# Performance work log

Hardware: AMD Instinct MI355X
Metric: run time of the kernel (lower is better)

## Reference

```python
import jax, jax.numpy as jnp
import numpy as np

B, S, D, H = 4, 1024, 1024, 16
DK = D // H


def setup_inputs() -> dict:
    key = jax.random.key(0)
    ks = jax.random.split(key, 13)
    s = 1.0 / np.sqrt(D)
    return {
        "query": jax.random.normal(ks[0], (B, S, D), jnp.float32),
        "key": jax.random.normal(ks[1], (B, S, D), jnp.float32),
        "value": jax.random.normal(ks[2], (B, S, D), jnp.float32),
        "mask": jax.random.randint(ks[3], (B, H, S, S), 0, 2).astype(bool),
        "Wq": jax.random.normal(ks[4], (D, D), jnp.float32) * s,
        "bq": jnp.zeros((D,), jnp.float32),
        "Wk": jax.random.normal(ks[5], (D, D), jnp.float32) * s,
        "bk": jnp.zeros((D,), jnp.float32),
        "Wv": jax.random.normal(ks[6], (D, D), jnp.float32) * s,
        "bv": jnp.zeros((D,), jnp.float32),
        "Wo": jax.random.normal(ks[7], (D, D), jnp.float32) * s,
        "bo": jnp.zeros((D,), jnp.float32),
    }


def reference(query, key, value, mask, Wq, bq, Wk, bk, Wv, bv, Wo, bo):
    b = query.shape[0]
    # QKV projections, split heads: [B,S,D] -> [B,H,S,DK]
    q = (query @ Wq + bq).reshape(b, -1, H, DK).transpose(0, 2, 1, 3)
    k = (key @ Wk + bk).reshape(b, -1, H, DK).transpose(0, 2, 1, 3)
    v = (value @ Wv + bv).reshape(b, -1, H, DK).transpose(0, 2, 1, 3)
    # scaled dot-product attention with explicit [B,H,Sq,Sk] scores
    scores = jnp.einsum("bhqd,bhkd->bhqk", q, k) / jnp.sqrt(jnp.float32(DK))
    scores = jnp.where(mask, -jnp.inf, scores)
    attn_weights = jax.nn.softmax(scores, axis=-1)
    attn_out = jnp.einsum("bhqk,bhkd->bhqd", attn_weights, v)
    # merge heads and project out; dropout is identity in eval mode
    attn_out = attn_out.transpose(0, 2, 1, 3).reshape(b, -1, D)
    out = attn_out @ Wo + bo
    return out, attn_weights
```

## Files before the change

kernel.cpp:

```cpp
#include <hip/hip_runtime.h>

typedef __attribute__((ext_vector_type(8))) __bf16   bf16x8;
typedef __attribute__((ext_vector_type(4))) __bf16   bf16x4;
typedef __attribute__((ext_vector_type(8))) _Float16 halfx8;
typedef __attribute__((ext_vector_type(4))) float    floatx4;
typedef __attribute__((ext_vector_type(4))) int      intx4;

#define S_  1024
#define D_  1024
#define H_  16
#define DK_ 64
#define B_  4
#define M_  4096

__device__ __forceinline__ void gload_lds16(const void* g, void* l) {
  __builtin_amdgcn_global_load_lds(
      (const __attribute__((address_space(1))) unsigned int*)g,
      (__attribute__((address_space(3))) unsigned int*)l, 16, 0, 0);
}

__global__ __launch_bounds__(256) void prep(
    const float* __restrict__ q, const float* __restrict__ k,
    const float* __restrict__ v, __bf16* __restrict__ X,
    const float* __restrict__ W0, const float* __restrict__ W1,
    const float* __restrict__ W2, const float* __restrict__ W3,
    __bf16* __restrict__ WT, const unsigned char* __restrict__ m,
    int* __restrict__ flag)
{
  __shared__ __align__(16) unsigned char shb[9216];
  const int bid = blockIdx.x;
  const int t = threadIdx.x;
  if (bid < 6144) {
    const int z = bid >> 11;
    const int bx = bid & 2047;
    const float* src = (z == 0) ? q : (z == 1) ? k : v;
    __bf16* dst = X + (size_t)z * 4194304;
    const size_t idx = ((size_t)bx * 256 + t) * 8;
    floatx4 a = *(const floatx4*)(src + idx);
    floatx4 b = *(const floatx4*)(src + idx + 4);
    bf16x8 o;
#pragma unroll
    for (int j = 0; j < 4; ++j) { o[j] = (__bf16)a[j]; o[4 + j] = (__bf16)b[j]; }
    *(bf16x8*)(dst + idx) = o;
  } else if (bid < 7168) {
    const int g = bid - 6144;
    const int z = g >> 8, yy = (g >> 4) & 15, xx = g & 15;
    const float* W = (z == 0) ? W0 : (z == 1) ? W1 : (z == 2) ? W2 : W3;
    __bf16* O = WT + (size_t)z * (D_ * (size_t)D_);
    __bf16* T = (__bf16*)shb;
    const int r0 = yy * 64, c0 = xx * 64;
#pragma unroll
    for (int it = 0; it < 4; ++it) {
      int idx = t * 4 + it * 1024;
      int r = idx >> 6, c = idx & 63;
      floatx4 a = *(const floatx4*)(W + (size_t)(r0 + r) * D_ + c0 + c);
      bf16x4 o;
#pragma unroll
      for (int j = 0; j < 4; ++j) o[j] = (__bf16)a[j];
      *(bf16x4*)(&T[r * 72 + c]) = o;
    }
    __syncthreads();
#pragma unroll
    for (int it = 0; it < 2; ++it) {
      int idx = t * 8 + it * 2048;
      int orow = idx >> 6, oc = idx & 63;
      bf16x8 vv;
#pragma unroll
      for (int j = 0; j < 8; ++j) vv[j] = T[(oc + j) * 72 + orow];
      *(bf16x8*)(O + (size_t)(c0 + orow) * D_ + (r0 + oc)) = vv;
    }
  } else {
    unsigned* sacc = (unsigned*)shb;
    unsigned acc = 0;
    for (int i = t; i < 4096; i += 256)
      if (i & 3) acc |= m[i];
    sacc[t] = acc;
    __syncthreads();
    if (t == 0) {
      unsigned tot = 0;
      for (int i = 0; i < 256; ++i) tot |= sacc[i];
      flag[0] = tot ? 1 : 0;
    }
  }
}

template <int MODE>
__device__ __forceinline__ void gemm_body(
    const __bf16* __restrict__ X, const __bf16* __restrict__ WT,
    const float* __restrict__ bias, void* __restrict__ outp, __bf16* sh,
    const int m0, const int n0)
{
  __bf16* As = sh;
  __bf16* Bs = sh + 128 * 64;
  const int t = threadIdx.x;
  const int w = t >> 6, lane = t & 63, quad = lane >> 4, cl = lane & 15;
  const int wm = w >> 1, wn = w & 1;
  const int srow = lane >> 3, scol = (lane & 7) * 8;

  floatx4 acc[4][4];
#pragma unroll
  for (int i = 0; i < 4; ++i)
#pragma unroll
    for (int j = 0; j < 4; ++j) acc[i][j] = (floatx4){0.f, 0.f, 0.f, 0.f};

  for (int kt = 0; kt < 16; ++kt) {
    const int k0 = kt * 64;
    __syncthreads();
#pragma unroll
    for (int it = 0; it < 4; ++it) {
      const int ch = it * 4 + w;
      gload_lds16(X  + (size_t)(m0 + ch * 8 + srow) * D_ + k0 + scol, As + ch * 512);
      gload_lds16(WT + (size_t)(n0 + ch * 8 + srow) * D_ + k0 + scol, Bs + ch * 512);
    }
    __syncthreads();
#pragma unroll
    for (int ks = 0; ks < 2; ++ks) {
      bf16x8 a[4], b[4];
#pragma unroll
      for (int mt = 0; mt < 4; ++mt)
        a[mt] = *(const bf16x8*)(&As[(wm * 64 + mt * 16 + cl) * 64 + ks * 32 + quad * 8]);
#pragma unroll
      for (int nt = 0; nt < 4; ++nt)
        b[nt] = *(const bf16x8*)(&Bs[(wn * 64 + nt * 16 + cl) * 64 + ks * 32 + quad * 8]);
#pragma unroll
      for (int mt = 0; mt < 4; ++mt)
#pragma unroll
        for (int nt = 0; nt < 4; ++nt)
          acc[mt][nt] = __builtin_amdgcn_mfma_f32_16x16x32_bf16(a[mt], b[nt], acc[mt][nt], 0, 0, 0);
    }
  }

  if (MODE <= 2) {
#pragma unroll
    for (int mt = 0; mt < 4; ++mt)
#pragma unroll
      for (int nt = 0; nt < 4; ++nt) {
        const int nl = n0 + wn * 64 + nt * 16 + cl;
        const float bv = bias[nl];
#pragma unroll
        for (int r = 0; r < 4; ++r) {
          const int ml = m0 + wm * 64 + mt * 16 + quad * 4 + r;
          float v = acc[mt][nt][r] + bv;
          if (MODE == 0) {
            ((float*)outp)[(size_t)ml * D_ + nl] = v;
          } else {
            if (MODE == 1) v *= 0.125f;
            const int bb = ml >> 10, ss = ml & 1023, hh = nl >> 6, dd = nl & 63;
            ((_Float16*)outp)[(size_t)((bb * H_ + hh) * S_ + ss) * DK_ + dd] = (_Float16)v;
          }
        }
      }
  } else {
    __syncthreads();
    __bf16* T = sh + w * (64 * 72);
    const int hbase = n0 + wn * 64;
#pragma unroll
    for (int mt = 0; mt < 4; ++mt)
#pragma unroll
      for (int nt = 0; nt < 4; ++nt) {
        const int nl = hbase + nt * 16 + cl;
        const float bv = bias[nl];
        const int dk = nt * 16 + cl;
#pragma unroll
        for (int r = 0; r < 4; ++r) {
          const int sl = mt * 16 + quad * 4 + r;
          T[dk * 72 + sl] = (__bf16)(acc[mt][nt][r] + bv);
        }
      }
    __syncthreads();
    const int bb = m0 >> 10;
    const int hh = hbase >> 6;
    __bf16* out = (__bf16*)outp;
#pragma unroll
    for (int i = 0; i < 8; ++i) {
      int idx = lane * 8 + i * 512;
      int dk = idx >> 6, sl = idx & 63;
      bf16x8 v = *(const bf16x8*)(&T[dk * 72 + sl]);
      int sg = (m0 & 1023) + wm * 64 + sl;
      *(bf16x8*)(out + (size_t)((bb * H_ + hh) * DK_ + dk) * S_ + sg) = v;
    }
  }
}

__global__ __launch_bounds__(256) void gemm_qkv(
    const __bf16* __restrict__ Xbf, const __bf16* __restrict__ wt,
    const float* __restrict__ bq, const float* __restrict__ bk,
    const float* __restrict__ bv,
    void* __restrict__ Qo, void* __restrict__ Ko, void* __restrict__ Vto)
{
  __shared__ __bf16 sh[18432];
  const int z = blockIdx.z;
  const int m0 = blockIdx.x * 128, n0 = blockIdx.y * 128;
  if (z == 0)      gemm_body<1>(Xbf,               wt,               bq, Qo,  sh, m0, n0);
  else if (z == 1) gemm_body<2>(Xbf + 4194304,     wt + 1048576,     bk, Ko,  sh, m0, n0);
  else             gemm_body<3>(Xbf + 2 * 4194304, wt + 2 * 1048576, bv, Vto, sh, m0, n0);
}

__global__ __launch_bounds__(256) void gemm_out(
    const __bf16* __restrict__ X, const __bf16* __restrict__ WT,
    const float* __restrict__ bias, float* __restrict__ outp)
{
  __shared__ __bf16 sh[18432];
  gemm_body<0>(X, WT, bias, (void*)outp, sh, blockIdx.x * 128, blockIdx.y * 128);
}

__global__ __launch_bounds__(256, 1) void attn_kernel(
    const _Float16* __restrict__ Q, const _Float16* __restrict__ K,
    const __bf16* __restrict__ Vt, const unsigned char* __restrict__ maskB,
    const int* __restrict__ mflag, float* __restrict__ attnW,
    __bf16* __restrict__ AO)
{
  __shared__ __align__(16) unsigned char smem[151296];
  __bf16*        P   = (__bf16*)smem;
  _Float16*      Qs  = (_Float16*)smem;
  _Float16*      Ks  = (_Float16*)(smem + 132096);
  __bf16*        Vts = (__bf16*)(smem + 141312);
  unsigned char* Ms  = smem + 150528;
  float*         rls = (float*)(smem + 151040);

  const int t = threadIdx.x;
  const int w = t >> 6, lane = t & 63, quad = lane >> 4, cl = lane & 15;
  const int o = blockIdx.x + blockIdx.y * 16;
  const int f = (o & 7) * 128 + (o >> 3);
  const int q0 = (f & 15) * 64;
  const int bh = f >> 4;
  const bool mbyte = (*mflag != 0);
  const int* maskI = (const int*)maskB;
  const long maskbase = (long)bh * S_ * S_;

  {
    const _Float16* g = Q + (size_t)(bh * S_ + q0) * DK_;
#pragma unroll
    for (int it = 0; it < 2; ++it) {
      int idx = t * 8 + it * 2048;
      *(halfx8*)(&Qs[(idx >> 6) * 72 + (idx & 63)]) = *(const halfx8*)(g + idx);
    }
  }

  halfx8 kreg0, kreg1;
  bf16x8 vreg0, vreg1;
  intx4  mregs[4];
  const _Float16* Kbase  = K  + (size_t)bh * S_ * DK_;
  const __bf16*   Vbase  = Vt + (size_t)bh * DK_ * S_;

#define LOAD_TILE(KT)                                                              \
  {                                                                                \
    const int k0_ = (KT) * 64;                                                     \
    const _Float16* gk = Kbase + (size_t)k0_ * DK_;                                \
    kreg0 = *(const halfx8*)(gk + t * 8);                                          \
    kreg1 = *(const halfx8*)(gk + t * 8 + 2048);                                   \
    const __bf16* gv = Vbase + k0_;                                                \
    vreg0 = *(const bf16x8*)(gv + (size_t)(t >> 3) * S_ + (t & 7) * 8);            \
    vreg1 = *(const bf16x8*)(gv + (size_t)((t >> 3) + 32) * S_ + (t & 7) * 8);     \
    if (mbyte) {                                                                   \
      mregs[0] = *(const intx4*)(maskB + maskbase +                                \
                   (size_t)(q0 + (t >> 2)) * S_ + k0_ + (t & 3) * 16);             \
    } else {                                                                       \
      const int* mrowp = maskI + maskbase + (size_t)(q0 + (t >> 2)) * S_ + k0_ +   \
                         (t & 3) * 16;                                             \
      _Pragma("unroll")                                                            \
      for (int it_ = 0; it_ < 4; ++it_)                                            \
        mregs[it_] = *(const intx4*)(mrowp + it_ * 4);                             \
    }                                                                              \
  }

  LOAD_TILE(0);
  __syncthreads();
  const halfx8 a0 = *(const halfx8*)(&Qs[(w * 16 + cl) * 72 + quad * 8]);
  const halfx8 a1 = *(const halfx8*)(&Qs[(w * 16 + cl) * 72 + 32 + quad * 8]);

  float lacc[4] = {0.f, 0.f, 0.f, 0.f};
  floatx4 acc_o[4];
#pragma unroll
  for (int i = 0; i < 4; ++i) acc_o[i] = (floatx4){0.f, 0.f, 0.f, 0.f};
  __bf16* Pw = P + (size_t)(w * 16) * 1032;

  for (int kt = 0; kt < 16; ++kt) {
    const int k0 = kt * 64;
    __syncthreads();

    *(halfx8*)(&Ks[(t >> 3) * 72 + (t & 7) * 8])        = kreg0;
    *(halfx8*)(&Ks[((t >> 3) + 32) * 72 + (t & 7) * 8]) = kreg1;
    *(bf16x8*)(&Vts[(t >> 3) * 72 + (t & 7) * 8])        = vreg0;
    *(bf16x8*)(&Vts[((t >> 3) + 32) * 72 + (t & 7) * 8]) = vreg1;
    {
      unsigned m16 = 0;
      if (mbyte) {
#pragma unroll
        for (int i = 0; i < 4; ++i) {
          unsigned v = (unsigned)mregs[0][i];
          m16 |= ((v & 0x000000ffu) ? 1u : 0u) << (i * 4 + 0);
          m16 |= ((v & 0x0000ff00u) ? 1u : 0u) << (i * 4 + 1);
          m16 |= ((v & 0x00ff0000u) ? 1u : 0u) << (i * 4 + 2);
          m16 |= ((v & 0xff000000u) ? 1u : 0u) << (i * 4 + 3);
        }
      } else {
#pragma unroll
        for (int it = 0; it < 4; ++it)
#pragma unroll
          for (int j = 0; j < 4; ++j)
            m16 |= (mregs[it][j] ? 1u : 0u) << (it * 4 + j);
      }
      ((unsigned short*)Ms)[(t >> 2) * 4 + (t & 3)] = (unsigned short)m16;
    }
    __syncthreads();

    unsigned long long mrow[4];
#pragma unroll
    for (int r = 0; r < 4; ++r)
      mrow[r] = ((const unsigned long long*)Ms)[w * 16 + quad * 4 + r];

    if (kt < 15) LOAD_TILE(kt + 1);

#pragma unroll
    for (int nt = 0; nt < 4; ++nt) {
      floatx4 s = (floatx4){0.f, 0.f, 0.f, 0.f};
      halfx8 b0 = *(const halfx8*)(&Ks[(nt * 16 + cl) * 72 + quad * 8]);
      halfx8 b1 = *(const halfx8*)(&Ks[(nt * 16 + cl) * 72 + 32 + quad * 8]);
      __builtin_amdgcn_s_setprio(1);
      s = __builtin_amdgcn_mfma_f32_16x16x32_f16(a0, b0, s, 0, 0, 0);
      s = __builtin_amdgcn_mfma_f32_16x16x32_f16(a1, b1, s, 0, 0, 0);
      __builtin_amdgcn_s_setprio(0);
#pragma unroll
      for (int r = 0; r < 4; ++r) {
        const int mk = (int)((mrow[r] >> (nt * 16 + cl)) & 1ull);
        float sv = s[r];
        sv = (sv < 25.f) ? sv : 25.f;
        float p = mk ? 0.0f : __expf(sv);
        __bf16 pb = (__bf16)p;
        lacc[r] += (float)pb;
        Pw[(quad * 4 + r) * 1032 + k0 + nt * 16 + cl] = pb;
      }
    }

    __builtin_amdgcn_s_setprio(1);
#pragma unroll
    for (int ks = 0; ks < 2; ++ks) {
      bf16x8 a = *(const bf16x8*)(&Pw[cl * 1032 + k0 + ks * 32 + quad * 8]);
#pragma unroll
      for (int nt2 = 0; nt2 < 4; ++nt2) {
        bf16x8 b = *(const bf16x8*)(&Vts[(nt2 * 16 + cl) * 72 + ks * 32 + quad * 8]);
        acc_o[nt2] = __builtin_amdgcn_mfma_f32_16x16x32_bf16(a, b, acc_o[nt2], 0, 0, 0);
      }
    }
    __builtin_amdgcn_s_setprio(0);
  }
#undef LOAD_TILE

  const int bb = bh >> 4, hh = bh & 15;
#pragma unroll
  for (int r = 0; r < 4; ++r) {
    float v = lacc[r];
    v += __shfl_xor(v, 1); v += __shfl_xor(v, 2);
    v += __shfl_xor(v, 4); v += __shfl_xor(v, 8);
    const int rowg = q0 + w * 16 + quad * 4 + r;
    const float rl = (v > 0.f) ? 1.0f / v : 0.f;
    if (cl == 0) rls[w * 16 + quad * 4 + r] = rl;
#pragma unroll
    for (int nt2 = 0; nt2 < 4; ++nt2) {
      float o2 = acc_o[nt2][r] * rl;
      AO[(size_t)(bb * S_ + rowg) * D_ + hh * DK_ + nt2 * 16 + cl] = (__bf16)o2;
    }
  }

  for (int rr = 0; rr < 16; ++rr) {
    const float rlv = rls[w * 16 + rr];
    float* g = attnW + ((size_t)(bh * S_) + q0 + w * 16 + rr) * S_;
    const __bf16* prow = &Pw[(size_t)rr * 1032];
#pragma unroll
    for (int i = 0; i < 4; ++i) {
      const int c = lane * 4 + i * 256;
      bf16x4 pv = *(const bf16x4*)(prow + c);
      floatx4 ov;
#pragma unroll
      for (int j = 0; j < 4; ++j) ov[j] = (float)pv[j] * rlv;
      *(floatx4*)(g + c) = ov;
    }
  }
}

extern "C" void kernel_launch(void* const* d_in, const int* in_sizes, int n_in,
                              void* d_out, int out_size, void* d_ws, size_t ws_size,
                              hipStream_t stream)
{
  (void)in_sizes; (void)n_in; (void)out_size; (void)ws_size;
  const float* query = (const float*)d_in[0];
  const float* key   = (const float*)d_in[1];
  const float* value = (const float*)d_in[2];
  const unsigned char* mask = (const unsigned char*)d_in[3];
  const float* Wq = (const float*)d_in[4];
  const float* bq = (const float*)d_in[5];
  const float* Wk = (const float*)d_in[6];
  const float* bk = (const float*)d_in[7];
  const float* Wv = (const float*)d_in[8];
  const float* bv = (const float*)d_in[9];
  const float* Wo = (const float*)d_in[10];
  const float* bo = (const float*)d_in[11];

  __bf16* ws = (__bf16*)d_ws;
  __bf16*   wt   = ws;
  _Float16* Qws  = (_Float16*)(ws + 4  * 1048576);
  _Float16* Kws  = (_Float16*)(ws + 8  * 1048576);
  __bf16*   Vtws = ws + 12 * 1048576;
  __bf16*   AOws = ws + 16 * 1048576;
  __bf16*   Xbf  = ws + 20 * 1048576;
  int*      mfl  = (int*)(ws + 32 * 1048576 + 131072);

  float* outO  = (float*)d_out;
  float* attnW = outO + 4 * 1048576;

  prep<<<7169, 256, 0, stream>>>(query, key, value, Xbf, Wq, Wk, Wv, Wo, wt, mask, mfl);
  gemm_qkv<<<dim3(32, 8, 3), 256, 0, stream>>>(Xbf, wt, bq, bk, bv,
                                               (void*)Qws, (void*)Kws, (void*)Vtws);
  attn_kernel<<<dim3(16, 64), 256, 0, stream>>>(Qws, Kws, Vtws, mask, mfl,
                                                attnW, AOws);
  gemm_out<<<dim3(32, 8), 256, 0, stream>>>(AOws, wt + 3 * 1048576, bo, outO);
}
```

Baseline: 622.6 us.

## Double attention waves per block by splitting key tiles across wave pairs

```diff
diff --git a/kernel.cpp b/kernel.cpp
--- a/kernel.cpp
+++ b/kernel.cpp
@@ -204,22 +204,24 @@
   gemm_body<0>(X, WT, bias, (void*)outp, sh, blockIdx.x * 128, blockIdx.y * 128);
 }
 
-__global__ __launch_bounds__(256, 1) void attn_kernel(
+__global__ __launch_bounds__(512, 1) void attn_kernel(
     const _Float16* __restrict__ Q, const _Float16* __restrict__ K,
     const __bf16* __restrict__ Vt, const unsigned char* __restrict__ maskB,
     const int* __restrict__ mflag, float* __restrict__ attnW,
     __bf16* __restrict__ AO)
 {
-  __shared__ __align__(16) unsigned char smem[151296];
+  __shared__ __align__(16) unsigned char smem[150784];
   __bf16*        P   = (__bf16*)smem;
   _Float16*      Qs  = (_Float16*)smem;
-  _Float16*      Ks  = (_Float16*)(smem + 132096);
-  __bf16*        Vts = (__bf16*)(smem + 141312);
-  unsigned char* Ms  = smem + 150528;
-  float*         rls = (float*)(smem + 151040);
+  _Float16*      Ks  = (_Float16*)(smem + 131328);
+  __bf16*        Vts = (__bf16*)(smem + 140544);
+  unsigned char* Ms  = smem + 149760;
+  float*         rls = (float*)(smem + 150272);
+  float*         S1  = (float*)(smem + 150528);
 
   const int t = threadIdx.x;
   const int w = t >> 6, lane = t & 63, quad = lane >> 4, cl = lane & 15;
+  const int wr = w & 3, wh = w >> 2;
   const int o = blockIdx.x + blockIdx.y * 16;
   const int f = (o & 7) * 128 + (o >> 3);
   const int q0 = (f & 15) * 64;
@@ -230,90 +232,83 @@
 
   {
     const _Float16* g = Q + (size_t)(bh * S_ + q0) * DK_;
-#pragma unroll
-    for (int it = 0; it < 2; ++it) {
-      int idx = t * 8 + it * 2048;
-      *(halfx8*)(&Qs[(idx >> 6) * 72 + (idx & 63)]) = *(const halfx8*)(g + idx);
-    }
-  }
-
-  halfx8 kreg0, kreg1;
-  bf16x8 vreg0, vreg1;
-  intx4  mregs[4];
+    const int idx = t * 8;
+    *(halfx8*)(&Qs[(idx >> 6) * 72 + (idx & 63)]) = *(const halfx8*)(g + idx);
+  }
+
+  halfx8 kreg;
+  bf16x8 vreg;
+  intx4  mra, mrb;
   const _Float16* Kbase  = K  + (size_t)bh * S_ * DK_;
   const __bf16*   Vbase  = Vt + (size_t)bh * DK_ * S_;
 
 #define LOAD_TILE(KT)                                                              \
   {                                                                                \
     const int k0_ = (KT) * 64;                                                     \
-    const _Float16* gk = Kbase + (size_t)k0_ * DK_;                                \
-    kreg0 = *(const halfx8*)(gk + t * 8);                                          \
-    kreg1 = *(const halfx8*)(gk + t * 8 + 2048);                                   \
-    const __bf16* gv = Vbase + k0_;                                                \
-    vreg0 = *(const bf16x8*)(gv + (size_t)(t >> 3) * S_ + (t & 7) * 8);            \
-    vreg1 = *(const bf16x8*)(gv + (size_t)((t >> 3) + 32) * S_ + (t & 7) * 8);     \
+    kreg = *(const halfx8*)(Kbase + (size_t)k0_ * DK_ + t * 8);                    \
+    vreg = *(const bf16x8*)(Vbase + (size_t)(t >> 3) * S_ + k0_ + (t & 7) * 8);    \
     if (mbyte) {                                                                   \
-      mregs[0] = *(const intx4*)(maskB + maskbase +                                \
-                   (size_t)(q0 + (t >> 2)) * S_ + k0_ + (t & 3) * 16);             \
+      int2 mv = *(const int2*)(maskB + maskbase +                                  \
+                   (size_t)(q0 + (t >> 3)) * S_ + k0_ + (t & 7) * 8);              \
+      mra.x = mv.x; mra.y = mv.y;                                                  \
     } else {                                                                       \
-      const int* mrowp = maskI + maskbase + (size_t)(q0 + (t >> 2)) * S_ + k0_ +   \
-                         (t & 3) * 16;                                             \
-      _Pragma("unroll")                                                            \
-      for (int it_ = 0; it_ < 4; ++it_)                                            \
-        mregs[it_] = *(const intx4*)(mrowp + it_ * 4);                             \
+      const int* mp = maskI + maskbase + (size_t)(q0 + (t >> 3)) * S_ + k0_ +      \
+                      (t & 7) * 8;                                                 \
+      mra = *(const intx4*)(mp);                                                   \
+      mrb = *(const intx4*)(mp + 4);                                               \
     }                                                                              \
   }
 
   LOAD_TILE(0);
   __syncthreads();
-  const halfx8 a0 = *(const halfx8*)(&Qs[(w * 16 + cl) * 72 + quad * 8]);
-  const halfx8 a1 = *(const halfx8*)(&Qs[(w * 16 + cl) * 72 + 32 + quad * 8]);
+  const halfx8 a0 = *(const halfx8*)(&Qs[(wr * 16 + cl) * 72 + quad * 8]);
+  const halfx8 a1 = *(const halfx8*)(&Qs[(wr * 16 + cl) * 72 + 32 + quad * 8]);
 
   float lacc[4] = {0.f, 0.f, 0.f, 0.f};
   floatx4 acc_o[4];
 #pragma unroll
   for (int i = 0; i < 4; ++i) acc_o[i] = (floatx4){0.f, 0.f, 0.f, 0.f};
-  __bf16* Pw = P + (size_t)(w * 16) * 1032;
+  __bf16* Pw = P + (size_t)(wr * 16) * 1026;
 
   for (int kt = 0; kt < 16; ++kt) {
     const int k0 = kt * 64;
     __syncthreads();
 
-    *(halfx8*)(&Ks[(t >> 3) * 72 + (t & 7) * 8])        = kreg0;
-    *(halfx8*)(&Ks[((t >> 3) + 32) * 72 + (t & 7) * 8]) = kreg1;
-    *(bf16x8*)(&Vts[(t >> 3) * 72 + (t & 7) * 8])        = vreg0;
-    *(bf16x8*)(&Vts[((t >> 3) + 32) * 72 + (t & 7) * 8]) = vreg1;
+    *(halfx8*)(&Ks[(t >> 3) * 72 + (t & 7) * 8]) = kreg;
+    *(bf16x8*)(&Vts[(t >> 3) * 72 + (t & 7) * 8]) = vreg;
     {
-      unsigned m16 = 0;
+      unsigned m8 = 0;
       if (mbyte) {
-#pragma unroll
-        for (int i = 0; i < 4; ++i) {
-          unsigned v = (unsigned)mregs[0][i];
-          m16 |= ((v & 0x000000ffu) ? 1u : 0u) << (i * 4 + 0);
-          m16 |= ((v & 0x0000ff00u) ? 1u : 0u) << (i * 4 + 1);
-          m16 |= ((v & 0x00ff0000u) ? 1u : 0u) << (i * 4 + 2);
-          m16 |= ((v & 0xff000000u) ? 1u : 0u) << (i * 4 + 3);
+        unsigned x = (unsigned)mra.x, y = (unsigned)mra.y;
+        m8 |= ((x & 0x000000ffu) ? 1u : 0u) << 0;
+        m8 |= ((x & 0x0000ff00u) ? 1u : 0u) << 1;
+        m8 |= ((x & 0x00ff0000u) ? 1u : 0u) << 2;
+        m8 |= ((x & 0xff000000u) ? 1u : 0u) << 3;
+        m8 |= ((y & 0x000000ffu) ? 1u : 0u) << 4;
+        m8 |= ((y & 0x0000ff00u) ? 1u : 0u) << 5;
+        m8 |= ((y & 0x00ff0000u) ? 1u : 0u) << 6;
+        m8 |= ((y & 0xff000000u) ? 1u : 0u) << 7;
+      } else {
+#pragma unroll
+        for (int j = 0; j < 4; ++j) {
+          m8 |= (mra[j] ? 1u : 0u) << j;
+          m8 |= (mrb[j] ? 1u : 0u) << (4 + j);
         }
-      } else {
-#pragma unroll
-        for (int it = 0; it < 4; ++it)
-#pragma unroll
-          for (int j = 0; j < 4; ++j)
-            m16 |= (mregs[it][j] ? 1u : 0u) << (it * 4 + j);
-      }
-      ((unsigned short*)Ms)[(t >> 2) * 4 + (t & 3)] = (unsigned short)m16;
+      }
+      Ms[(t >> 3) * 8 + (t & 7)] = (unsigned char)m8;
     }
     __syncthreads();
 
     unsigned long long mrow[4];
 #pragma unroll
     for (int r = 0; r < 4; ++r)
-      mrow[r] = ((const unsigned long long*)Ms)[w * 16 + quad * 4 + r];
+      mrow[r] = ((const unsigned long long*)Ms)[wr * 16 + quad * 4 + r];
 
     if (kt < 15) LOAD_TILE(kt + 1);
 
 #pragma unroll
-    for (int nt = 0; nt < 4; ++nt) {
+    for (int ntl = 0; ntl < 2; ++ntl) {
+      const int nt = wh * 2 + ntl;
       floatx4 s = (floatx4){0.f, 0.f, 0.f, 0.f};
       halfx8 b0 = *(const halfx8*)(&Ks[(nt * 16 + cl) * 72 + quad * 8]);
       halfx8 b1 = *(const halfx8*)(&Ks[(nt * 16 + cl) * 72 + 32 + quad * 8]);
@@ -329,17 +324,16 @@
         float p = mk ? 0.0f : __expf(sv);
         __bf16 pb = (__bf16)p;
         lacc[r] += (float)pb;
-        Pw[(quad * 4 + r) * 1032 + k0 + nt * 16 + cl] = pb;
+        Pw[(quad * 4 + r) * 1026 + k0 + nt * 16 + cl] = pb;
       }
     }
 
     __builtin_amdgcn_s_setprio(1);
-#pragma unroll
-    for (int ks = 0; ks < 2; ++ks) {
-      bf16x8 a = *(const bf16x8*)(&Pw[cl * 1032 + k0 + ks * 32 + quad * 8]);
+    {
+      bf16x8 a = *(const bf16x8*)(&Pw[cl * 1026 + k0 + wh * 32 + quad * 8]);
 #pragma unroll
       for (int nt2 = 0; nt2 < 4; ++nt2) {
-        bf16x8 b = *(const bf16x8*)(&Vts[(nt2 * 16 + cl) * 72 + ks * 32 + quad * 8]);
+        bf16x8 b = *(const bf16x8*)(&Vts[(nt2 * 16 + cl) * 72 + wh * 32 + quad * 8]);
         acc_o[nt2] = __builtin_amdgcn_mfma_f32_16x16x32_bf16(a, b, acc_o[nt2], 0, 0, 0);
       }
     }
@@ -347,26 +341,54 @@
   }
 #undef LOAD_TILE
 
-  const int bb = bh >> 4, hh = bh & 15;
-#pragma unroll
-  for (int r = 0; r < 4; ++r) {
-    float v = lacc[r];
-    v += __shfl_xor(v, 1); v += __shfl_xor(v, 2);
-    v += __shfl_xor(v, 4); v += __shfl_xor(v, 8);
-    const int rowg = q0 + w * 16 + quad * 4 + r;
-    const float rl = (v > 0.f) ? 1.0f / v : 0.f;
-    if (cl == 0) rls[w * 16 + quad * 4 + r] = rl;
-#pragma unroll
-    for (int nt2 = 0; nt2 < 4; ++nt2) {
-      float o2 = acc_o[nt2][r] * rl;
-      AO[(size_t)(bb * S_ + rowg) * D_ + hh * DK_ + nt2 * 16 + cl] = (__bf16)o2;
-    }
-  }
-
-  for (int rr = 0; rr < 16; ++rr) {
-    const float rlv = rls[w * 16 + rr];
-    float* g = attnW + ((size_t)(bh * S_) + q0 + w * 16 + rr) * S_;
-    const __bf16* prow = &Pw[(size_t)rr * 1032];
+  __syncthreads();
+  float* Xo = (float*)(smem + 131328);
+  if (wh == 1) {
+#pragma unroll
+    for (int nt2 = 0; nt2 < 4; ++nt2)
+#pragma unroll
+      for (int j = 0; j < 4; ++j)
+        Xo[(wr * 64 + lane) * 16 + nt2 * 4 + j] = acc_o[nt2][j];
+#pragma unroll
+    for (int r = 0; r < 4; ++r) {
+      float v = lacc[r];
+      v += __shfl_xor(v, 1); v += __shfl_xor(v, 2);
+      v += __shfl_xor(v, 4); v += __shfl_xor(v, 8);
+      if (cl == 0) S1[wr * 16 + quad * 4 + r] = v;
+    }
+  }
+  __syncthreads();
+  if (wh == 0) {
+    const int bb = bh >> 4, hh = bh & 15;
+#pragma unroll
+    for (int nt2 = 0; nt2 < 4; ++nt2)
+#pragma unroll
+      for (int j = 0; j < 4; ++j)
+        acc_o[nt2][j] += Xo[(wr * 64 + lane) * 16 + nt2 * 4 + j];
+#pragma unroll
+    for (int r = 0; r < 4; ++r) {
+      float v = lacc[r];
+      v += __shfl_xor(v, 1); v += __shfl_xor(v, 2);
+      v += __shfl_xor(v, 4); v += __shfl_xor(v, 8);
+      v += S1[wr * 16 + quad * 4 + r];
+      const int rowg = q0 + wr * 16 + quad * 4 + r;
+      const float rl = (v > 0.f) ? 1.0f / v : 0.f;
+      if (cl == 0) rls[wr * 16 + quad * 4 + r] = rl;
+#pragma unroll
+      for (int nt2 = 0; nt2 < 4; ++nt2) {
+        float o2 = acc_o[nt2][r] * rl;
+        AO[(size_t)(bb * S_ + rowg) * D_ + hh * DK_ + nt2 * 16 + cl] = (__bf16)o2;
+      }
+    }
+  }
+  __syncthreads();
+
+#pragma unroll
+  for (int rr = 0; rr < 8; ++rr) {
+    const int row = w * 8 + rr;
+    const float rlv = rls[row];
+    float* g = attnW + ((size_t)(bh * S_) + q0 + row) * S_;
+    const __bf16* prow = &P[(size_t)row * 1026];
 #pragma unroll
     for (int i = 0; i < 4; ++i) {
       const int c = lane * 4 + i * 256;
@@ -412,7 +434,7 @@
   prep<<<7169, 256, 0, stream>>>(query, key, value, Xbf, Wq, Wk, Wv, Wo, wt, mask, mfl);
   gemm_qkv<<<dim3(32, 8, 3), 256, 0, stream>>>(Xbf, wt, bq, bk, bv,
                                                (void*)Qws, (void*)Kws, (void*)Vtws);
-  attn_kernel<<<dim3(16, 64), 256, 0, stream>>>(Qws, Kws, Vtws, mask, mfl,
+  attn_kernel<<<dim3(16, 64), 512, 0, stream>>>(Qws, Kws, Vtws, mask, mfl,
                                                 attnW, AOws);
   gemm_out<<<dim3(32, 8), 256, 0, stream>>>(AOws, wt + 3 * 1048576, bo, outO);
 }
```

After: 620.7 us. No clear change (-0.3%).
